# Performance work log

Hardware: AMD Instinct MI355X
Metric: run time of the kernel (lower is better)

Reference implementation:

```python
import jax, jax.numpy as jnp
import numpy as np

B, T, C = 2, 4096, 512
H = 8
MEMORY = 256  # window: key j visible to query i iff 0 <= i - j <= MEMORY


def setup_inputs() -> dict:
    key = jax.random.key(0)
    k1, k2, k3 = jax.random.split(key, 3)
    x = jax.random.normal(k1, (B, T, C), dtype=jnp.float32)
    w_attn = jax.random.normal(k2, (3 * C, C), dtype=jnp.float32) * 0.02
    w_proj = jax.random.normal(k3, (C, C), dtype=jnp.float32) * 0.02
    return {"x": x, "w_attn": w_attn, "w_proj": w_proj}


def reference(x, w_attn, w_proj):
    b, t, c = x.shape
    d = c // H
    # fused QKV projection (Linear without bias): x @ W^T
    qkv = jnp.einsum('btc,fc->btf', x, w_attn)  # [B,T,3C]
    q, k, v = jnp.split(qkv, 3, axis=-1)
    # [B,T,C] -> [B,H,T,d]
    q = q.reshape(b, t, H, d).transpose(0, 2, 1, 3)
    k = k.reshape(b, t, H, d).transpose(0, 2, 1, 3)
    v = v.reshape(b, t, H, d).transpose(0, 2, 1, 3)
    # sliding-window causal mask: tril(0) & ~tril(-memory-1)
    i = jnp.arange(t)[:, None]
    j = jnp.arange(t)[None, :]
    mask = (j <= i) & (i - j <= MEMORY)  # [T,T] bool
    scores = jnp.einsum('bhqd,bhkd->bhqk', q, k) * (1.0 / np.sqrt(d))
    scores = jnp.where(mask, scores, -jnp.inf)
    attn = jax.nn.softmax(scores, axis=-1)
    y = jnp.einsum('bhqk,bhkd->bhqd', attn, v)  # [B,H,T,d]
    y = y.transpose(0, 2, 1, 3).reshape(b, t, c)
    # output projection
    y = jnp.einsum('btc,fc->btf', y, w_proj)
    return y
```

## Files before the change

### kernel.cpp

```cpp
#include <hip/hip_runtime.h>
#include <hip/hip_bf16.h>
#include <stdint.h>

#define BB 2
#define TT 4096
#define CC 512
#define HH 8
#define MEM 256

typedef unsigned short u16;
typedef __bf16 bf16x8 __attribute__((ext_vector_type(8)));
typedef float floatx4 __attribute__((ext_vector_type(4)));

__device__ inline u16 f2bf(float f) {
  uint32_t u = __float_as_uint(f);
  uint32_t r = (u + 0x7fffu + ((u >> 16) & 1u)) >> 16;
  return (u16)r;
}
__device__ inline u16 f2bf_r(float f) {
  return (u16)((__float_as_uint(f) + 0x8000u) >> 16);
}

__device__ inline void gld16(const u16* g, u16* lds) {
  __builtin_amdgcn_global_load_lds(
      (const __attribute__((address_space(1))) uint32_t*)g,
      (__attribute__((address_space(3))) uint32_t*)lds, 16, 0, 0);
}

__global__ __launch_bounds__(256) void cvt_all(const float* __restrict__ x,
                                               const float* __restrict__ wa,
                                               const float* __restrict__ wp,
                                               u16* __restrict__ xb,
                                               u16* __restrict__ wab,
                                               u16* __restrict__ wpb) {
  int i = blockIdx.x * 256 + threadIdx.x;
  const float* s; u16* d; int off;
  if (i < 1048576) { s = x; d = xb; off = i; }
  else if (i < 1245184) { s = wa; d = wab; off = i - 1048576; }
  else { s = wp; d = wpb; off = i - 1245184; }
  float4 v = *reinterpret_cast<const float4*>(s + (size_t)off * 4);
  ushort4 o;
  o.x = f2bf(v.x); o.y = f2bf(v.y); o.z = f2bf(v.z); o.w = f2bf(v.w);
  *reinterpret_cast<ushort4*>(d + (size_t)off * 4) = o;
}

__global__ __launch_bounds__(256, 4) void gemm_qkv(const u16* __restrict__ A,
                                                   const u16* __restrict__ Bw,
                                                   u16* __restrict__ Cout,
                                                   int M, int N, int K) {
  __shared__ __align__(16) u16 As[128 * 64];
  __shared__ __align__(16) u16 Bs[64 * 64];
  const int tid = threadIdx.x;
  const int w = tid >> 6, lane = tid & 63, quad = lane >> 4, l16 = lane & 15;
  const int m0 = blockIdx.y * 128, n0 = blockIdx.x * 64;

  floatx4 acc[2][4] = {};
  const int nK = K >> 6;
  for (int kb = 0; kb < nK; ++kb) {
    const int kof = kb * 64;
#pragma unroll
    for (int j = 0; j < 4; j++) {
      int c = tid + j * 256, row = c >> 3, blk = (c & 7) ^ (row & 7);
      gld16(A + (size_t)(m0 + row) * K + kof + blk * 8, As + (size_t)c * 8);
    }
#pragma unroll
    for (int j = 0; j < 2; j++) {
      int c = tid + j * 256, row = c >> 3, blk = (c & 7) ^ (row & 7);
      gld16(Bw + (size_t)(n0 + row) * K + kof + blk * 8, Bs + (size_t)c * 8);
    }
    __syncthreads();
#pragma unroll
    for (int half = 0; half < 2; ++half) {
      bf16x8 af[2], bfr[4];
#pragma unroll
      for (int i = 0; i < 2; i++)
        af[i] = *reinterpret_cast<const bf16x8*>(
            &As[(w * 32 + i * 16 + l16) * 64 + (((half << 2) | quad) ^ (l16 & 7)) * 8]);
#pragma unroll
      for (int i = 0; i < 4; i++)
        bfr[i] = *reinterpret_cast<const bf16x8*>(
            &Bs[(i * 16 + l16) * 64 + (((half << 2) | quad) ^ (l16 & 7)) * 8]);
#pragma unroll
      for (int mi = 0; mi < 2; mi++)
#pragma unroll
        for (int ni = 0; ni < 4; ni++)
          acc[mi][ni] = __builtin_amdgcn_mfma_f32_16x16x32_bf16(af[mi], bfr[ni], acc[mi][ni], 0, 0, 0);
    }
    __syncthreads();
  }
#pragma unroll
  for (int mi = 0; mi < 2; mi++)
#pragma unroll
    for (int ni = 0; ni < 4; ni++)
#pragma unroll
      for (int r = 0; r < 4; r++)
        As[(w * 32 + mi * 16 + quad * 4 + r) * 64 + ni * 16 + l16] = f2bf(acc[mi][ni][r]);
  __syncthreads();
#pragma unroll
  for (int p = 0; p < 4; p++) {
    int idx = p * 2048 + tid * 8;
    int row = idx >> 6, col = idx & 63;
    *reinterpret_cast<uint4*>(&Cout[(size_t)(m0 + row) * N + n0 + col]) =
        *reinterpret_cast<const uint4*>(&As[idx]);
  }
}

__global__ __launch_bounds__(256, 4) void gemm_proj(const u16* __restrict__ A,
                                                    const u16* __restrict__ Bw,
                                                    float* __restrict__ C,
                                                    int M, int N, int K) {
  __shared__ __align__(16) u16 As[64 * 64];
  __shared__ __align__(16) u16 Bs[64 * 64];
  const int tid = threadIdx.x;
  const int w = tid >> 6, lane = tid & 63, quad = lane >> 4, l16 = lane & 15;
  const int wm = w >> 1, wn = w & 1;
  const int m0 = blockIdx.y * 64, n0 = blockIdx.x * 64;

  floatx4 acc[2][2] = {};
  const int nK = K >> 6;
  for (int kb = 0; kb < nK; ++kb) {
    const int kof = kb * 64;
#pragma unroll
    for (int j = 0; j < 2; j++) {
      int c = tid + j * 256, row = c >> 3, blk = (c & 7) ^ (row & 7);
      gld16(A + (size_t)(m0 + row) * K + kof + blk * 8, As + (size_t)c * 8);
    }
#pragma unroll
    for (int j = 0; j < 2; j++) {
      int c = tid + j * 256, row = c >> 3, blk = (c & 7) ^ (row & 7);
      gld16(Bw + (size_t)(n0 + row) * K + kof + blk * 8, Bs + (size_t)c * 8);
    }
    __syncthreads();
#pragma unroll
    for (int half = 0; half < 2; ++half) {
      bf16x8 af[2], bfr[2];
#pragma unroll
      for (int i = 0; i < 2; i++)
        af[i] = *reinterpret_cast<const bf16x8*>(
            &As[(wm * 32 + i * 16 + l16) * 64 + (((half << 2) | quad) ^ (l16 & 7)) * 8]);
#pragma unroll
      for (int i = 0; i < 2; i++)
        bfr[i] = *reinterpret_cast<const bf16x8*>(
            &Bs[(wn * 32 + i * 16 + l16) * 64 + (((half << 2) | quad) ^ (l16 & 7)) * 8]);
#pragma unroll
      for (int mi = 0; mi < 2; mi++)
#pragma unroll
        for (int ni = 0; ni < 2; ni++)
          acc[mi][ni] = __builtin_amdgcn_mfma_f32_16x16x32_bf16(af[mi], bfr[ni], acc[mi][ni], 0, 0, 0);
    }
    __syncthreads();
  }
#pragma unroll
  for (int mi = 0; mi < 2; mi++) {
    int row = m0 + wm * 32 + mi * 16 + quad * 4;
#pragma unroll
    for (int ni = 0; ni < 2; ni++) {
      int col = n0 + wn * 32 + ni * 16 + l16;
#pragma unroll
      for (int r = 0; r < 4; r++)
        C[(size_t)(row + r) * N + col] = acc[mi][ni][r];
    }
  }
}

__global__ __launch_bounds__(256, 2) void attn_win(const u16* __restrict__ qkv,
                                                   u16* __restrict__ y) {
  const int q0 = blockIdx.x * 128;
  const int h = blockIdx.y;
  const int b = blockIdx.z;
  const int tid = threadIdx.x;
  const int w = tid >> 6, lane = tid & 63, quad = lane >> 4, l16 = lane & 15;

  __shared__ __align__(16) u16 Qs[128 * 64];
  __shared__ __align__(16) u16 Ks[64 * 64];
  __shared__ __align__(16) u16 Vt[64 * 72];
  __shared__ __align__(16) u16 Ps[4][32 * 72];

  const size_t baseQ = ((size_t)(b * TT + q0)) * 1536 + h * 64;
#pragma unroll
  for (int j = 0; j < 4; j++) {
    int c = tid + j * 256, row = c >> 3, blk = (c & 7) ^ (row & 7);
    gld16(qkv + baseQ + (size_t)row * 1536 + blk * 8, Qs + (size_t)c * 8);
  }
  __syncthreads();
  bf16x8 qf[2][2];
#pragma unroll
  for (int mi = 0; mi < 2; mi++) {
    int row = w * 32 + mi * 16 + l16;
    qf[mi][0] = *reinterpret_cast<const bf16x8*>(&Qs[row * 64 + (quad ^ (l16 & 7)) * 8]);
    qf[mi][1] = *reinterpret_cast<const bf16x8*>(&Qs[row * 64 + ((quad + 4) ^ (l16 & 7)) * 8]);
#pragma unroll
    for (int e = 0; e < 8; e++) {
      qf[mi][0][e] = qf[mi][0][e] * (__bf16)0.125f;
      qf[mi][1][e] = qf[mi][1][e] * (__bf16)0.125f;
    }
  }

  floatx4 acc_o[2][4] = {};
  float l_acc[2][4] = {{0.f, 0.f, 0.f, 0.f}, {0.f, 0.f, 0.f, 0.f}};

  const int s_min = (q0 >= 256) ? 0 : ((256 - q0) >> 6);
  const int key_v = tid >> 3, dc_v = tid & 7;
  const int key_v1 = (tid + 256) >> 3, dc_v1 = tid & 7;

  uint4 vp0, vp1;
  {
    size_t baseV = ((size_t)(b * TT + (q0 - 256 + s_min * 64))) * 1536 + 1024 + h * 64;
    vp0 = *reinterpret_cast<const uint4*>(qkv + baseV + (size_t)key_v * 1536 + dc_v * 8);
    vp1 = *reinterpret_cast<const uint4*>(qkv + baseV + (size_t)key_v1 * 1536 + dc_v1 * 8);
  }

  for (int s = s_min; s < 6; ++s) {
    const int k0 = q0 - 256 + s * 64;
    const size_t baseK = ((size_t)(b * TT + k0)) * 1536 + 512 + h * 64;
    {
      int c = tid, row = c >> 3, blk = (c & 7) ^ (row & 7);
      gld16(qkv + baseK + (size_t)row * 1536 + blk * 8, Ks + (size_t)c * 8);
      c = tid + 256; row = c >> 3; blk = (c & 7) ^ (row & 7);
      gld16(qkv + baseK + (size_t)row * 1536 + blk * 8, Ks + (size_t)c * 8);
    }
    {
      u16 tmp[8];
      *reinterpret_cast<uint4*>(tmp) = vp0;
      int col = key_v ^ (dc_v * 8);
#pragma unroll
      for (int e = 0; e < 8; e++) Vt[(dc_v * 8 + e) * 72 + col] = tmp[e];
      *reinterpret_cast<uint4*>(tmp) = vp1;
      col = key_v1 ^ (dc_v1 * 8);
#pragma unroll
      for (int e = 0; e < 8; e++) Vt[(dc_v1 * 8 + e) * 72 + col] = tmp[e];
    }
    if (s < 5) {
      size_t baseV = ((size_t)(b * TT + k0 + 64)) * 1536 + 1024 + h * 64;
      vp0 = *reinterpret_cast<const uint4*>(qkv + baseV + (size_t)key_v * 1536 + dc_v * 8);
      vp1 = *reinterpret_cast<const uint4*>(qkv + baseV + (size_t)key_v1 * 1536 + dc_v1 * 8);
    }
    __syncthreads();

    int mode = 0;
    if (s == 0) mode = (w < 2) ? 1 : 3;
    else if (s == 1) mode = (w < 2) ? 0 : 1;
    else if (s == 4) mode = (w < 2) ? 2 : 0;
    else if (s == 5) mode = (w < 2) ? 3 : 2;

    if (mode != 3) {
      bf16x8 bfr[4][2];
#pragma unroll
      for (int nt = 0; nt < 4; nt++) {
        int krow = nt * 16 + l16;
        bfr[nt][0] = *reinterpret_cast<const bf16x8*>(&Ks[krow * 64 + (quad ^ (l16 & 7)) * 8]);
        bfr[nt][1] = *reinterpret_cast<const bf16x8*>(&Ks[krow * 64 + ((quad + 4) ^ (l16 & 7)) * 8]);
      }
      floatx4 sc[2][4] = {};
#pragma unroll
      for (int mi = 0; mi < 2; mi++)
#pragma unroll
        for (int nt = 0; nt < 4; nt++) {
          sc[mi][nt] = __builtin_amdgcn_mfma_f32_16x16x32_bf16(qf[mi][0], bfr[nt][0], sc[mi][nt], 0, 0, 0);
          sc[mi][nt] = __builtin_amdgcn_mfma_f32_16x16x32_bf16(qf[mi][1], bfr[nt][1], sc[mi][nt], 0, 0, 0);
        }
      const int hqb = (w & 1) * 32 + quad * 4;
      if (mode == 1) {
#pragma unroll
        for (int mi = 0; mi < 2; mi++)
#pragma unroll
          for (int nt = 0; nt < 4; nt++)
#pragma unroll
            for (int r = 0; r < 4; r++)
              if (hqb + mi * 16 + r > nt * 16 + l16) sc[mi][nt][r] = -1e30f;
      } else if (mode == 2) {
#pragma unroll
        for (int mi = 0; mi < 2; mi++)
#pragma unroll
          for (int nt = 0; nt < 4; nt++)
#pragma unroll
            for (int r = 0; r < 4; r++)
              if (hqb + mi * 16 + r < nt * 16 + l16) sc[mi][nt][r] = -1e30f;
      }
#pragma unroll
      for (int mi = 0; mi < 2; mi++)
#pragma unroll
        for (int nt = 0; nt < 4; nt++)
#pragma unroll
          for (int r = 0; r < 4; r++) {
            float p = __expf(sc[mi][nt][r] - 4.0f);
            l_acc[mi][r] += p;
            Ps[w][(mi * 16 + quad * 4 + r) * 72 + nt * 16 + l16] = f2bf_r(p);
          }
#pragma unroll
      for (int mi = 0; mi < 2; mi++)
#pragma unroll
        for (int ki = 0; ki < 2; ki++) {
          bf16x8 pf = *reinterpret_cast<const bf16x8*>(
              &Ps[w][(mi * 16 + l16) * 72 + ki * 32 + quad * 8]);
#pragma unroll
          for (int nt = 0; nt < 4; nt++) {
            int d = nt * 16 + l16;
            bf16x8 vf = *reinterpret_cast<const bf16x8*>(
                &Vt[d * 72 + ((ki * 32 + quad * 8) ^ (d & 56))]);
            acc_o[mi][nt] = __builtin_amdgcn_mfma_f32_16x16x32_bf16(pf, vf, acc_o[mi][nt], 0, 0, 0);
          }
        }
    }
    __syncthreads();
  }
#pragma unroll
  for (int mi = 0; mi < 2; mi++)
#pragma unroll
    for (int r = 0; r < 4; r++) {
      float l = l_acc[mi][r];
      l += __shfl_xor(l, 1);
      l += __shfl_xor(l, 2);
      l += __shfl_xor(l, 4);
      l += __shfl_xor(l, 8);
      float inv = 1.f / l;
      int row = q0 + w * 32 + mi * 16 + quad * 4 + r;
      size_t base = (size_t)(b * TT + row) * 512 + h * 64;
#pragma unroll
      for (int nt = 0; nt < 4; nt++)
        y[base + nt * 16 + l16] = f2bf(acc_o[mi][nt][r] * inv);
    }
}

extern "C" void kernel_launch(void* const* d_in, const int* in_sizes, int n_in,
                              void* d_out, int out_size, void* d_ws, size_t ws_size,
                              hipStream_t stream) {
  const float* x = (const float*)d_in[0];
  const float* w_attn = (const float*)d_in[1];
  const float* w_proj = (const float*)d_in[2];
  float* out = (float*)d_out;

  u16* xb = (u16*)d_ws;
  u16* wab = xb + (size_t)8192 * 512;
  u16* wpb = wab + (size_t)1536 * 512;
  u16* qkv = wpb + (size_t)512 * 512;
  u16* yb = qkv + (size_t)8192 * 1536;

  cvt_all<<<5120, 256, 0, stream>>>(x, w_attn, w_proj, xb, wab, wpb);
  gemm_qkv<<<dim3(24, 64), 256, 0, stream>>>(xb, wab, qkv, 8192, 1536, 512);
  attn_win<<<dim3(TT / 128, HH, BB), 256, 0, stream>>>(qkv, yb);
  gemm_proj<<<dim3(8, 128), 256, 0, stream>>>(yb, wpb, out, 8192, 512, 512);
}
```

Baseline: 127.2 us.

## Fuse fp32-to-bf16 conversion into GEMMs and emit head-major Q/K and transposed V

Drops the separate conversion kernel. The GEMMs now load fp32 inputs and convert them to bf16 while staging into LDS. The QKV GEMM writes Q (pre-scaled by 1/8) and K in head-major layout and V transposed per head. This lets the attention kernel use contiguous async LDS loads instead of a register-staged manual V transpose. The cost is that GEMM operand loads go through registers (fp32, twice the bytes) rather than direct global-to-LDS, and the weights are reconverted by every block.

```diff
diff --git a/kernel.cpp b/kernel.cpp
--- a/kernel.cpp
+++ b/kernel.cpp
@@ -27,27 +27,20 @@
       (__attribute__((address_space(3))) uint32_t*)lds, 16, 0, 0);
 }
 
-__global__ __launch_bounds__(256) void cvt_all(const float* __restrict__ x,
-                                               const float* __restrict__ wa,
-                                               const float* __restrict__ wp,
-                                               u16* __restrict__ xb,
-                                               u16* __restrict__ wab,
-                                               u16* __restrict__ wpb) {
-  int i = blockIdx.x * 256 + threadIdx.x;
-  const float* s; u16* d; int off;
-  if (i < 1048576) { s = x; d = xb; off = i; }
-  else if (i < 1245184) { s = wa; d = wab; off = i - 1048576; }
-  else { s = wp; d = wpb; off = i - 1245184; }
-  float4 v = *reinterpret_cast<const float4*>(s + (size_t)off * 4);
-  ushort4 o;
-  o.x = f2bf(v.x); o.y = f2bf(v.y); o.z = f2bf(v.z); o.w = f2bf(v.w);
-  *reinterpret_cast<ushort4*>(d + (size_t)off * 4) = o;
-}
-
-__global__ __launch_bounds__(256, 4) void gemm_qkv(const u16* __restrict__ A,
-                                                   const u16* __restrict__ Bw,
-                                                   u16* __restrict__ Cout,
-                                                   int M, int N, int K) {
+__device__ inline void ld8_cvt(const float* src, u16* dst_lds) {
+  float4 a = *reinterpret_cast<const float4*>(src);
+  float4 b = *reinterpret_cast<const float4*>(src + 4);
+  u16 t[8];
+  t[0] = f2bf(a.x); t[1] = f2bf(a.y); t[2] = f2bf(a.z); t[3] = f2bf(a.w);
+  t[4] = f2bf(b.x); t[5] = f2bf(b.y); t[6] = f2bf(b.z); t[7] = f2bf(b.w);
+  *reinterpret_cast<uint4*>(dst_lds) = *reinterpret_cast<const uint4*>(t);
+}
+
+__global__ __launch_bounds__(256, 4) void gemm_qkv(const float* __restrict__ x,
+                                                   const float* __restrict__ wa,
+                                                   u16* __restrict__ qh,
+                                                   u16* __restrict__ kh,
+                                                   u16* __restrict__ vt) {
   __shared__ __align__(16) u16 As[128 * 64];
   __shared__ __align__(16) u16 Bs[64 * 64];
   const int tid = threadIdx.x;
@@ -55,18 +48,17 @@
   const int m0 = blockIdx.y * 128, n0 = blockIdx.x * 64;
 
   floatx4 acc[2][4] = {};
-  const int nK = K >> 6;
-  for (int kb = 0; kb < nK; ++kb) {
+  for (int kb = 0; kb < 8; ++kb) {
     const int kof = kb * 64;
 #pragma unroll
     for (int j = 0; j < 4; j++) {
       int c = tid + j * 256, row = c >> 3, blk = (c & 7) ^ (row & 7);
-      gld16(A + (size_t)(m0 + row) * K + kof + blk * 8, As + (size_t)c * 8);
+      ld8_cvt(x + (size_t)(m0 + row) * 512 + kof + blk * 8, As + (size_t)c * 8);
     }
 #pragma unroll
     for (int j = 0; j < 2; j++) {
       int c = tid + j * 256, row = c >> 3, blk = (c & 7) ^ (row & 7);
-      gld16(Bw + (size_t)(n0 + row) * K + kof + blk * 8, Bs + (size_t)c * 8);
+      ld8_cvt(wa + (size_t)(n0 + row) * 512 + kof + blk * 8, Bs + (size_t)c * 8);
     }
     __syncthreads();
 #pragma unroll
@@ -88,27 +80,47 @@
     }
     __syncthreads();
   }
-#pragma unroll
-  for (int mi = 0; mi < 2; mi++)
-#pragma unroll
-    for (int ni = 0; ni < 4; ni++)
-#pragma unroll
-      for (int r = 0; r < 4; r++)
-        As[(w * 32 + mi * 16 + quad * 4 + r) * 64 + ni * 16 + l16] = f2bf(acc[mi][ni][r]);
-  __syncthreads();
-#pragma unroll
-  for (int p = 0; p < 4; p++) {
-    int idx = p * 2048 + tid * 8;
-    int row = idx >> 6, col = idx & 63;
-    *reinterpret_cast<uint4*>(&Cout[(size_t)(m0 + row) * N + n0 + col]) =
-        *reinterpret_cast<const uint4*>(&As[idx]);
+  const int type = n0 >> 9;
+  const int h = (n0 >> 6) & 7;
+  const int b = m0 >> 12, t0 = m0 & 4095;
+  if (type == 2) {
+    const size_t bv = ((size_t)(b * 8 + h)) * 64 * 4096;
+#pragma unroll
+    for (int mi = 0; mi < 2; mi++)
+#pragma unroll
+      for (int ni = 0; ni < 4; ni++) {
+        int d = ni * 16 + l16;
+        int t = t0 + w * 32 + mi * 16 + quad * 4;
+        uint32_t p0 = (uint32_t)f2bf(acc[mi][ni][0]) | ((uint32_t)f2bf(acc[mi][ni][1]) << 16);
+        uint32_t p1 = (uint32_t)f2bf(acc[mi][ni][2]) | ((uint32_t)f2bf(acc[mi][ni][3]) << 16);
+        uint2 pk = {p0, p1};
+        *reinterpret_cast<uint2*>(&vt[bv + (size_t)d * 4096 + t]) = pk;
+      }
+  } else {
+    u16* dst = (type == 0) ? qh : kh;
+    const float sc = (type == 0) ? 0.125f : 1.0f;
+#pragma unroll
+    for (int mi = 0; mi < 2; mi++)
+#pragma unroll
+      for (int ni = 0; ni < 4; ni++)
+#pragma unroll
+        for (int r = 0; r < 4; r++)
+          As[(w * 32 + mi * 16 + quad * 4 + r) * 64 + ni * 16 + l16] =
+              f2bf(acc[mi][ni][r] * sc);
+    __syncthreads();
+    const size_t base = ((size_t)(b * 8 + h) * 4096 + t0) * 64;
+#pragma unroll
+    for (int p = 0; p < 4; p++) {
+      int idx = p * 2048 + tid * 8;
+      *reinterpret_cast<uint4*>(&dst[base + idx]) =
+          *reinterpret_cast<const uint4*>(&As[idx]);
+    }
   }
 }
 
 __global__ __launch_bounds__(256, 4) void gemm_proj(const u16* __restrict__ A,
-                                                    const u16* __restrict__ Bw,
-                                                    float* __restrict__ C,
-                                                    int M, int N, int K) {
+                                                    const float* __restrict__ wp,
+                                                    float* __restrict__ C) {
   __shared__ __align__(16) u16 As[64 * 64];
   __shared__ __align__(16) u16 Bs[64 * 64];
   const int tid = threadIdx.x;
@@ -117,18 +129,17 @@
   const int m0 = blockIdx.y * 64, n0 = blockIdx.x * 64;
 
   floatx4 acc[2][2] = {};
-  const int nK = K >> 6;
-  for (int kb = 0; kb < nK; ++kb) {
+  for (int kb = 0; kb < 8; ++kb) {
     const int kof = kb * 64;
 #pragma unroll
     for (int j = 0; j < 2; j++) {
       int c = tid + j * 256, row = c >> 3, blk = (c & 7) ^ (row & 7);
-      gld16(A + (size_t)(m0 + row) * K + kof + blk * 8, As + (size_t)c * 8);
+      gld16(A + (size_t)(m0 + row) * 512 + kof + blk * 8, As + (size_t)c * 8);
     }
 #pragma unroll
     for (int j = 0; j < 2; j++) {
       int c = tid + j * 256, row = c >> 3, blk = (c & 7) ^ (row & 7);
-      gld16(Bw + (size_t)(n0 + row) * K + kof + blk * 8, Bs + (size_t)c * 8);
+      ld8_cvt(wp + (size_t)(n0 + row) * 512 + kof + blk * 8, Bs + (size_t)c * 8);
     }
     __syncthreads();
 #pragma unroll
@@ -158,12 +169,14 @@
       int col = n0 + wn * 32 + ni * 16 + l16;
 #pragma unroll
       for (int r = 0; r < 4; r++)
-        C[(size_t)(row + r) * N + col] = acc[mi][ni][r];
-    }
-  }
-}
-
-__global__ __launch_bounds__(256, 2) void attn_win(const u16* __restrict__ qkv,
+        C[(size_t)(row + r) * 512 + col] = acc[mi][ni][r];
+    }
+  }
+}
+
+__global__ __launch_bounds__(256, 2) void attn_win(const u16* __restrict__ qh,
+                                                   const u16* __restrict__ kh,
+                                                   const u16* __restrict__ vt,
                                                    u16* __restrict__ y) {
   const int q0 = blockIdx.x * 128;
   const int h = blockIdx.y;
@@ -173,14 +186,15 @@
 
   __shared__ __align__(16) u16 Qs[128 * 64];
   __shared__ __align__(16) u16 Ks[64 * 64];
-  __shared__ __align__(16) u16 Vt[64 * 72];
+  __shared__ __align__(16) u16 Vt[64 * 64];
   __shared__ __align__(16) u16 Ps[4][32 * 72];
 
-  const size_t baseQ = ((size_t)(b * TT + q0)) * 1536 + h * 64;
+  const size_t hb = (size_t)(b * 8 + h);
+  const size_t bq = (hb * 4096 + q0) * 64;
 #pragma unroll
   for (int j = 0; j < 4; j++) {
     int c = tid + j * 256, row = c >> 3, blk = (c & 7) ^ (row & 7);
-    gld16(qkv + baseQ + (size_t)row * 1536 + blk * 8, Qs + (size_t)c * 8);
+    gld16(qh + bq + (size_t)row * 64 + blk * 8, Qs + (size_t)c * 8);
   }
   __syncthreads();
   bf16x8 qf[2][2];
@@ -189,51 +203,27 @@
     int row = w * 32 + mi * 16 + l16;
     qf[mi][0] = *reinterpret_cast<const bf16x8*>(&Qs[row * 64 + (quad ^ (l16 & 7)) * 8]);
     qf[mi][1] = *reinterpret_cast<const bf16x8*>(&Qs[row * 64 + ((quad + 4) ^ (l16 & 7)) * 8]);
-#pragma unroll
-    for (int e = 0; e < 8; e++) {
-      qf[mi][0][e] = qf[mi][0][e] * (__bf16)0.125f;
-      qf[mi][1][e] = qf[mi][1][e] * (__bf16)0.125f;
-    }
   }
 
   floatx4 acc_o[2][4] = {};
   float l_acc[2][4] = {{0.f, 0.f, 0.f, 0.f}, {0.f, 0.f, 0.f, 0.f}};
 
   const int s_min = (q0 >= 256) ? 0 : ((256 - q0) >> 6);
-  const int key_v = tid >> 3, dc_v = tid & 7;
-  const int key_v1 = (tid + 256) >> 3, dc_v1 = tid & 7;
-
-  uint4 vp0, vp1;
-  {
-    size_t baseV = ((size_t)(b * TT + (q0 - 256 + s_min * 64))) * 1536 + 1024 + h * 64;
-    vp0 = *reinterpret_cast<const uint4*>(qkv + baseV + (size_t)key_v * 1536 + dc_v * 8);
-    vp1 = *reinterpret_cast<const uint4*>(qkv + baseV + (size_t)key_v1 * 1536 + dc_v1 * 8);
-  }
-
   for (int s = s_min; s < 6; ++s) {
     const int k0 = q0 - 256 + s * 64;
-    const size_t baseK = ((size_t)(b * TT + k0)) * 1536 + 512 + h * 64;
+    const size_t bk = (hb * 4096 + k0) * 64;
     {
       int c = tid, row = c >> 3, blk = (c & 7) ^ (row & 7);
-      gld16(qkv + baseK + (size_t)row * 1536 + blk * 8, Ks + (size_t)c * 8);
+      gld16(kh + bk + (size_t)row * 64 + blk * 8, Ks + (size_t)c * 8);
       c = tid + 256; row = c >> 3; blk = (c & 7) ^ (row & 7);
-      gld16(qkv + baseK + (size_t)row * 1536 + blk * 8, Ks + (size_t)c * 8);
-    }
+      gld16(kh + bk + (size_t)row * 64 + blk * 8, Ks + (size_t)c * 8);
+    }
+    const size_t bv = hb * 64 * 4096;
     {
-      u16 tmp[8];
-      *reinterpret_cast<uint4*>(tmp) = vp0;
-      int col = key_v ^ (dc_v * 8);
-#pragma unroll
-      for (int e = 0; e < 8; e++) Vt[(dc_v * 8 + e) * 72 + col] = tmp[e];
-      *reinterpret_cast<uint4*>(tmp) = vp1;
-      col = key_v1 ^ (dc_v1 * 8);
-#pragma unroll
-      for (int e = 0; e < 8; e++) Vt[(dc_v1 * 8 + e) * 72 + col] = tmp[e];
-    }
-    if (s < 5) {
-      size_t baseV = ((size_t)(b * TT + k0 + 64)) * 1536 + 1024 + h * 64;
-      vp0 = *reinterpret_cast<const uint4*>(qkv + baseV + (size_t)key_v * 1536 + dc_v * 8);
-      vp1 = *reinterpret_cast<const uint4*>(qkv + baseV + (size_t)key_v1 * 1536 + dc_v1 * 8);
+      int c = tid, d = c >> 3, blk = (c & 7) ^ (d & 7);
+      gld16(vt + bv + (size_t)d * 4096 + k0 + blk * 8, Vt + (size_t)c * 8);
+      c = tid + 256; d = c >> 3; blk = (c & 7) ^ (d & 7);
+      gld16(vt + bv + (size_t)d * 4096 + k0 + blk * 8, Vt + (size_t)c * 8);
     }
     __syncthreads();
 
@@ -297,7 +287,7 @@
           for (int nt = 0; nt < 4; nt++) {
             int d = nt * 16 + l16;
             bf16x8 vf = *reinterpret_cast<const bf16x8*>(
-                &Vt[d * 72 + ((ki * 32 + quad * 8) ^ (d & 56))]);
+                &Vt[d * 64 + ((((ki << 2) | quad)) ^ (l16 & 7)) * 8]);
             acc_o[mi][nt] = __builtin_amdgcn_mfma_f32_16x16x32_bf16(pf, vf, acc_o[mi][nt], 0, 0, 0);
           }
         }
@@ -330,14 +320,12 @@
   const float* w_proj = (const float*)d_in[2];
   float* out = (float*)d_out;
 
-  u16* xb = (u16*)d_ws;
-  u16* wab = xb + (size_t)8192 * 512;
-  u16* wpb = wab + (size_t)1536 * 512;
-  u16* qkv = wpb + (size_t)512 * 512;
-  u16* yb = qkv + (size_t)8192 * 1536;
-
-  cvt_all<<<5120, 256, 0, stream>>>(x, w_attn, w_proj, xb, wab, wpb);
-  gemm_qkv<<<dim3(24, 64), 256, 0, stream>>>(xb, wab, qkv, 8192, 1536, 512);
-  attn_win<<<dim3(TT / 128, HH, BB), 256, 0, stream>>>(qkv, yb);
-  gemm_proj<<<dim3(8, 128), 256, 0, stream>>>(yb, wpb, out, 8192, 512, 512);
-}
+  u16* qh = (u16*)d_ws;
+  u16* kh = qh + (size_t)8192 * 512;
+  u16* vt = kh + (size_t)8192 * 512;
+  u16* yb = vt + (size_t)8192 * 512;
+
+  gemm_qkv<<<dim3(24, 64), 256, 0, stream>>>(x, w_attn, qh, kh, vt);
+  attn_win<<<dim3(TT / 128, HH, BB), 256, 0, stream>>>(qh, kh, vt, yb);
+  gemm_proj<<<dim3(8, 128), 256, 0, stream>>>(yb, w_proj, out);
+}
```

After: 136.5 us. 1.07x slower.
